# Optimization experiments

Hardware: AMD Instinct MI355X
Metric: run time of the kernel (lower is better)

The kernel has to match this reference:

```python
import jax, jax.numpy as jnp
import numpy as np
import math

B, C, N, M = 4, 128, 4096, 4096

def setup_inputs() -> dict:
    key = jax.random.key(0)
    ks = jax.random.split(key, 8)
    return {
        "x1": jax.random.normal(ks[0], (B, C, N), dtype=jnp.float32),
        "p1": jax.random.normal(ks[1], (B, 3, N), dtype=jnp.float32),
        "x2": jax.random.normal(ks[2], (B, C, M), dtype=jnp.float32),
        "p2": jax.random.normal(ks[3], (B, 3, M), dtype=jnp.float32),
        "Wq": jax.random.normal(ks[4], (C, C), dtype=jnp.float32) * 0.05,
        "Wk": jax.random.normal(ks[5], (C, C), dtype=jnp.float32) * 0.05,
        "Wv": jax.random.normal(ks[6], (C, C), dtype=jnp.float32) * 0.05,
        "Wpos": jax.random.normal(ks[7], (C, 3), dtype=jnp.float32) * 0.05,
    }

def reference(x1, p1, x2, p2, Wq, Wk, Wv, Wpos):
    # Conv1d with kernel_size=1, no bias == per-point matmul over channel dim.
    # NOTE: original forward uses self.pos for BOTH p1 and p2 (pos1 conv unused).
    pos = jnp.einsum('ck,bkn->bcn', Wpos, p1)   # [B,C,N]
    pos1 = jnp.einsum('ck,bkm->bcm', Wpos, p2)  # [B,C,M]
    q = jnp.einsum('dc,bcn->bdn', Wq, x1 + pos)   # [B,C,N]
    k = jnp.einsum('dc,bcm->bdm', Wk, x2 + pos1)  # [B,C,M]
    v = jnp.einsum('dc,bcm->bdm', Wv, x2)         # [B,C,M]
    scale = math.sqrt(q.shape[1])  # sqrt(C) -- q.shape[-2] in (B,C,N) layout
    energy = jnp.einsum('bcn,bcm->bnm', q, k) / scale  # [B,N,M]
    attention = jax.nn.softmax(energy, axis=-1)
    vout = jnp.einsum('bnm,bcm->bnc', attention, v)    # [B,N,C]
    out = jnp.swapaxes(vout, 1, 2) + x1                # [B,C,N] residual
    return jnp.swapaxes(out, 1, 2)                     # [B,N,C]
```

## Files before the change

### kernel.cpp

```cpp
#include <hip/hip_runtime.h>
#include <hip/hip_bf16.h>

#define B_ 4
#define C_ 128
#define N_ 4096
#define M_ 4096

typedef __bf16 bf16;
typedef __bf16 bf16x8 __attribute__((ext_vector_type(8)));
typedef float f32x4 __attribute__((ext_vector_type(4)));
typedef float f32x16 __attribute__((ext_vector_type(16)));

#define MFMA16(a, b, c) __builtin_amdgcn_mfma_f32_16x16x32_bf16(a, b, c, 0, 0, 0)
#define MFMA32(a, b, c) __builtin_amdgcn_mfma_f32_32x32x16_bf16(a, b, c, 0, 0, 0)

__device__ inline void gll16(const bf16* g, bf16* l) {
    __builtin_amdgcn_global_load_lds(
        (const __attribute__((address_space(1))) void*)g,
        (__attribute__((address_space(3))) void*)l, 16, 0, 0);
}

__device__ inline unsigned cvtpk(float a, float b) {
    unsigned r;
    asm("v_cvt_pk_bf16_f32 %0, %1, %2" : "=v"(r) : "v"(a), "v"(b));
    return r;
}

__global__ __launch_bounds__(256) void wcvt_kernel(
    const float* __restrict__ Wq, const float* __restrict__ Wk,
    const float* __restrict__ Wv, bf16* __restrict__ Wb) {
    int i = (blockIdx.x * 256 + threadIdx.x) * 4;
    const float* src = (i < 16384) ? Wq : (i < 32768) ? Wk : Wv;
    int off = i & 16383;
    float4 v = *(const float4*)(src + off);
    union { ushort4 u4; bf16 h[4]; } pk;
    pk.h[0] = (bf16)v.x; pk.h[1] = (bf16)v.y;
    pk.h[2] = (bf16)v.z; pk.h[3] = (bf16)v.w;
    *(ushort4*)(Wb + i) = pk.u4;
}

__global__ __launch_bounds__(768) void proj_kernel(
    const float* __restrict__ x1, const float* __restrict__ p1,
    const float* __restrict__ x2, const float* __restrict__ p2,
    const bf16* __restrict__ Wb, const float* __restrict__ Wpos,
    bf16* __restrict__ Qt, bf16* __restrict__ Kt, bf16* __restrict__ Vt) {
    __shared__ __align__(16) bf16 xp1[64 * 136];
    __shared__ __align__(16) bf16 xp2[64 * 136];
    __shared__ __align__(16) bf16 xr2[64 * 136];
    __shared__ float pp1[3 * 64], pp2[3 * 64], wls[384];

    const int t = threadIdx.x;
    const int b = blockIdx.y;
    const int n0 = blockIdx.x * 64;

    if (t < 48) {
        int k3 = t / 16, i4 = (t & 15) * 4;
        *(float4*)&pp1[k3 * 64 + i4] = *(const float4*)(p1 + ((size_t)b * 3 + k3) * N_ + n0 + i4);
    } else if (t < 96) {
        int tt = t - 48;
        int k3 = tt / 16, i4 = (tt & 15) * 4;
        *(float4*)&pp2[k3 * 64 + i4] = *(const float4*)(p2 + ((size_t)b * 3 + k3) * N_ + n0 + i4);
    } else if (t < 192) {
        int i4 = (t - 96) * 4;
        *(float4*)&wls[i4] = *(const float4*)(Wpos + i4);
    }
    __syncthreads();

    for (int s = t; s < 2048; s += 768) {
        int c = s >> 4, n4 = (s & 15) * 4;
        float4 xv = *(const float4*)(x1 + ((size_t)b * C_ + c) * N_ + n0 + n4);
        float w0 = wls[c * 3 + 0], w1 = wls[c * 3 + 1], w2 = wls[c * 3 + 2];
        const float* xa = &xv.x;
        #pragma unroll
        for (int j = 0; j < 4; ++j) {
            float pos = w0 * pp1[n4 + j] + w1 * pp1[64 + n4 + j] + w2 * pp1[128 + n4 + j];
            xp1[(n4 + j) * 136 + c] = (bf16)(xa[j] + pos);
        }
    }
    for (int s = t; s < 2048; s += 768) {
        int c = s >> 4, n4 = (s & 15) * 4;
        float4 xv = *(const float4*)(x2 + ((size_t)b * C_ + c) * N_ + n0 + n4);
        float w0 = wls[c * 3 + 0], w1 = wls[c * 3 + 1], w2 = wls[c * 3 + 2];
        const float* xa = &xv.x;
        #pragma unroll
        for (int j = 0; j < 4; ++j) {
            float pos = w0 * pp2[n4 + j] + w1 * pp2[64 + n4 + j] + w2 * pp2[128 + n4 + j];
            xp2[(n4 + j) * 136 + c] = (bf16)(xa[j] + pos);
            xr2[(n4 + j) * 136 + c] = (bf16)xa[j];
        }
    }
    __syncthreads();

    const int w = t >> 6;
    const int lane = t & 63;
    const int col = lane & 15, quad = lane >> 4;
    const int role = w >> 2, band = w & 3;
    const int nl = band * 16 + col;
    const int n = n0 + nl;

    const bf16* src = (role == 0) ? xp1 : (role == 1) ? xp2 : xr2;
    const bf16* Wm = Wb + role * 16384;

    bf16x8 bx[4];
    #pragma unroll
    for (int cs = 0; cs < 4; ++cs)
        bx[cs] = *(const bf16x8*)&src[nl * 136 + cs * 32 + quad * 8];

    #pragma unroll
    for (int dt = 0; dt < 8; ++dt) {
        f32x4 acc = {0.f, 0.f, 0.f, 0.f};
        #pragma unroll
        for (int cs = 0; cs < 4; ++cs) {
            bf16x8 wf = *(const bf16x8*)(Wm + (dt * 16 + col) * 128 + cs * 32 + quad * 8);
            acc = MFMA16(wf, bx[cs], acc);
        }
        if (role < 2) {
            bf16* Ot = (role == 0) ? Qt : Kt;
            union { ushort4 u4; bf16 h[4]; } pk;
            #pragma unroll
            for (int r = 0; r < 4; ++r) pk.h[r] = (bf16)acc[r];
            *(ushort4*)(Ot + ((size_t)b * N_ + n) * C_ + dt * 16 + quad * 4) = pk.u4;
        } else {
            #pragma unroll
            for (int r = 0; r < 4; ++r)
                Vt[((size_t)b * C_ + dt * 16 + quad * 4 + r) * (size_t)M_ + n] = (bf16)acc[r];
        }
    }
}

__global__ __launch_bounds__(512) void attn_kernel(
    const bf16* __restrict__ Qt, const bf16* __restrict__ Kt,
    const bf16* __restrict__ Vt, const float* __restrict__ x1,
    float* __restrict__ out) {
    __shared__ __align__(16) char smem[132096];

    const int t = threadIdx.x;
    const int w = t >> 6;
    const int lane = t & 63;
    const int col = lane & 31;
    const int hi = lane >> 5;
    const int kg = w & 3;
    const int qg = w >> 2;

    const int g0 = blockIdx.x;
    const int xcd = g0 & 7;
    const int b = xcd >> 1;
    const int qt = (xcd & 1) + ((g0 >> 3) << 1);
    const int n0 = qt * 64;

    const float KS = 0.12752107168406815f;

    const bf16* Kbase = Kt + (size_t)b * M_ * C_;
    const bf16* Vbase = Vt + (size_t)b * C_ * M_;

    bf16x8 qf[8];
    {
        const bf16* Qb = Qt + ((size_t)b * N_ + n0 + qg * 32 + col) * C_ + hi * 8;
        #pragma unroll
        for (int cs = 0; cs < 8; ++cs)
            qf[cs] = *(const bf16x8*)(Qb + cs * 16);
    }

    f32x16 oacc[4];
    #pragma unroll
    for (int i = 0; i < 4; ++i)
        #pragma unroll
        for (int j = 0; j < 16; ++j) oacc[i][j] = 0.f;
    float lacc = 0.f;

    const int key_l = (kg << 5) + col;
    const int kxor = (key_l & 15) << 4;

    const bf16* kpp[4];
    const bf16* vpp[4];
    #pragma unroll
    for (int i = 0; i < 4; ++i) {
        int g = ((w << 2) + i) * 64 + lane;
        int row = g >> 4;
        int sp = (g & 15) ^ (row & 15);
        kpp[i] = Kbase + (size_t)row * C_ + sp * 8;
        vpp[i] = Vbase + (size_t)row * M_ + sp * 8;
    }

    auto stageK = [&](char* dst) {
        #pragma unroll
        for (int i = 0; i < 4; ++i) {
            gll16(kpp[i], (bf16*)dst + ((w << 2) + i) * 512);
            kpp[i] += 128 * C_;
        }
    };
    auto stageV = [&](char* dst) {
        #pragma unroll
        for (int i = 0; i < 4; ++i) {
            gll16(vpp[i], (bf16*)dst + ((w << 2) + i) * 512);
            vpp[i] += 128;
        }
    };

    stageK(smem);
    stageV(smem + 65536);
    stageK(smem + 32768);

    f32x16 sA0, sA1, sB0, sB1;

    auto qkc = [&](const char* kbBuf, f32x16& T0, f32x16& T1) {
        #pragma unroll
        for (int q = 0; q < 16; ++q) { T0[q] = 0.f; T1[q] = 0.f; }
        const char* kbp = kbBuf + key_l * 256;
        __builtin_amdgcn_s_setprio(1);
        #pragma unroll
        for (int cs = 0; cs < 4; ++cs) {
            bf16x8 kf = *(const bf16x8*)(kbp + ((((cs << 1) + hi) << 4) ^ kxor));
            T0 = MFMA32(kf, qf[cs], T0);
        }
        #pragma unroll
        for (int cs = 4; cs < 8; ++cs) {
            bf16x8 kf = *(const bf16x8*)(kbp + ((((cs << 1) + hi) << 4) ^ kxor));
            T1 = MFMA32(kf, qf[cs], T1);
        }
        __builtin_amdgcn_s_setprio(0);
    };

    auto smpv = [&](f32x16& S0, f32x16& S1, const char* vbBuf) {
        float p[16];
        #pragma unroll
        for (int r = 0; r < 16; ++r) {
            float e = fminf((S0[r] + S1[r]) * KS, 60.f);
            p[r] = __builtin_amdgcn_exp2f(e);
        }
        {
            float s01 = (p[0] + p[1]) + (p[2] + p[3]);
            float s23 = (p[4] + p[5]) + (p[6] + p[7]);
            float s45 = (p[8] + p[9]) + (p[10] + p[11]);
            float s67 = (p[12] + p[13]) + (p[14] + p[15]);
            lacc += (s01 + s23) + (s45 + s67);
        }
        unsigned W0 = cvtpk(p[0], p[1]),  W1 = cvtpk(p[2], p[3]);
        unsigned W2 = cvtpk(p[4], p[5]),  W3 = cvtpk(p[6], p[7]);
        unsigned W4 = cvtpk(p[8], p[9]),  W5 = cvtpk(p[10], p[11]);
        unsigned W6 = cvtpk(p[12], p[13]), W7 = cvtpk(p[14], p[15]);
        unsigned X0 = hi ? W0 : W2, X1 = hi ? W1 : W3;
        unsigned Y0 = hi ? W4 : W6, Y1 = hi ? W5 : W7;
        X0 = __shfl_xor(X0, 32, 64);  X1 = __shfl_xor(X1, 32, 64);
        Y0 = __shfl_xor(Y0, 32, 64);  Y1 = __shfl_xor(Y1, 32, 64);
        uint4 u0, u1;
        u0.x = hi ? X0 : W0;  u0.y = hi ? X1 : W1;
        u0.z = hi ? W2 : X0;  u0.w = hi ? W3 : X1;
        u1.x = hi ? Y0 : W4;  u1.y = hi ? Y1 : W5;
        u1.z = hi ? W6 : Y0;  u1.w = hi ? W7 : Y1;
        bf16x8 af0 = __builtin_bit_cast(bf16x8, u0);
        bf16x8 af1 = __builtin_bit_cast(bf16x8, u1);

        __builtin_amdgcn_s_setprio(1);
        #pragma unroll
        for (int ct = 0; ct < 4; ++ct) {
            int c = (ct << 5) + col;
            const char* vbp = vbBuf + c * 256;
            int vxor = (c & 15) << 4;
            bf16x8 vf0 = *(const bf16x8*)(vbp + ((((kg << 2) + hi) << 4) ^ vxor));
            bf16x8 vf1 = *(const bf16x8*)(vbp + ((((kg << 2) + 2 + hi) << 4) ^ vxor));
            oacc[ct] = MFMA32(af0, vf0, oacc[ct]);
            oacc[ct] = MFMA32(af1, vf1, oacc[ct]);
        }
        __builtin_amdgcn_s_setprio(0);
    };

    asm volatile("s_waitcnt vmcnt(8)" ::: "memory");
    __builtin_amdgcn_sched_barrier(0);
    __builtin_amdgcn_s_barrier();
    __builtin_amdgcn_sched_barrier(0);
    qkc(smem, sA0, sA1);

    for (int jp = 0; jp < 16; ++jp) {
        const int j0 = jp * 2, j1 = j0 + 1;

        asm volatile("s_waitcnt vmcnt(0)" ::: "memory");
        __builtin_amdgcn_sched_barrier(0);
        __builtin_amdgcn_s_barrier();
        __builtin_amdgcn_sched_barrier(0);
        if (j0 < 31) stageV(smem + 98304);
        if (j0 < 30) stageK(smem);
        if (j0 < 31) qkc(smem + 32768, sB0, sB1);
        smpv(sA0, sA1, smem + 65536);
        asm volatile("s_waitcnt lgkmcnt(0)" ::: "memory");
        __builtin_amdgcn_sched_barrier(0);

        asm volatile("s_waitcnt vmcnt(0)" ::: "memory");
        __builtin_amdgcn_sched_barrier(0);
        __builtin_amdgcn_s_barrier();
        __builtin_amdgcn_sched_barrier(0);
        if (j1 < 31) stageV(smem + 65536);
        if (j1 < 30) stageK(smem + 32768);
        if (j1 < 31) qkc(smem, sA0, sA1);
        smpv(sB0, sB1, smem + 98304);
        asm volatile("s_waitcnt lgkmcnt(0)" ::: "memory");
        __builtin_amdgcn_sched_barrier(0);
    }

    __builtin_amdgcn_s_barrier();

    float* obuf = (float*)smem;
    float* lps  = (float*)(smem + 131072);

    lacc += __shfl_xor(lacc, 32, 64);
    if (hi == 0) lps[(kg << 6) + (qg << 5) + col] = lacc;

    #pragma unroll
    for (int ct = 0; ct < 4; ++ct)
        #pragma unroll
        for (int r = 0; r < 16; ++r) {
            int q = (r & 3) + ((r >> 2) << 3) + (hi << 2);
            obuf[kg * 8192 + ((qg << 5) + q) * 128 + (ct << 5) + col] = oacc[ct][r];
        }
    __syncthreads();

    const int c2 = lane << 1;
    #pragma unroll
    for (int j = 0; j < 8; ++j) {
        int q = (w << 3) + j;
        float s0 = 0.f, s1 = 0.f;
        #pragma unroll
        for (int pp = 0; pp < 4; ++pp) {
            float2 v = *(const float2*)&obuf[pp * 8192 + q * 128 + c2];
            s0 += v.x; s1 += v.y;
        }
        float lsum = lps[q] + lps[64 + q] + lps[128 + q] + lps[192 + q];
        float linv = 1.0f / lsum;
        int n = n0 + q;
        float o0 = s0 * linv + x1[((size_t)b * C_ + c2) * N_ + n];
        float o1 = s1 * linv + x1[((size_t)b * C_ + c2 + 1) * N_ + n];
        *(float2*)&out[((size_t)b * N_ + n) * C_ + c2] = make_float2(o0, o1);
    }
}

extern "C" void kernel_launch(void* const* d_in, const int* in_sizes, int n_in,
                              void* d_out, int out_size, void* d_ws, size_t ws_size,
                              hipStream_t stream) {
    const float* x1   = (const float*)d_in[0];
    const float* p1   = (const float*)d_in[1];
    const float* x2   = (const float*)d_in[2];
    const float* p2   = (const float*)d_in[3];
    const float* Wq   = (const float*)d_in[4];
    const float* Wk   = (const float*)d_in[5];
    const float* Wv   = (const float*)d_in[6];
    const float* Wpos = (const float*)d_in[7];
    float* out = (float*)d_out;

    bf16* Qt = (bf16*)d_ws;
    bf16* Kt = Qt + (size_t)B_ * N_ * C_;
    bf16* Vt = Kt + (size_t)B_ * M_ * C_;

    bf16* Wb = (bf16*)d_out;

    wcvt_kernel<<<dim3(48), dim3(256), 0, stream>>>(Wq, Wk, Wv, Wb);
    proj_kernel<<<dim3(64, B_), dim3(768), 0, stream>>>(
        x1, p1, x2, p2, Wb, Wpos, Qt, Kt, Vt);
    attn_kernel<<<dim3(256), dim3(512), 0, stream>>>(Qt, Kt, Vt, x1, out);
}
```

Baseline: 143.9 us.

## Split projection kernel into per-role blocks via grid z dimension

The Q/K/V projection kernel now launches a separate 256-thread block for each of Q, K and V instead of one 768-thread block that computes all three. Each block stages only its own input tile in shared memory, so shared-memory use per block drops and more blocks can run at once. The x2 tile is now loaded twice, once by the K blocks and once by the V blocks. For Q and K the MFMA operands are swapped, so each lane writes single bf16 values at stride C instead of packed 4-element stores, which may scatter the global writes.

Measured after the change: 143.8 us. About the same (-0.0%).

```diff
diff --git a/kernel.cpp b/kernel.cpp
--- a/kernel.cpp
+++ b/kernel.cpp
@@ -39,54 +39,51 @@
     *(ushort4*)(Wb + i) = pk.u4;
 }
 
-__global__ __launch_bounds__(768) void proj_kernel(
+__global__ __launch_bounds__(256) void proj_kernel(
     const float* __restrict__ x1, const float* __restrict__ p1,
     const float* __restrict__ x2, const float* __restrict__ p2,
     const bf16* __restrict__ Wb, const float* __restrict__ Wpos,
     bf16* __restrict__ Qt, bf16* __restrict__ Kt, bf16* __restrict__ Vt) {
-    __shared__ __align__(16) bf16 xp1[64 * 136];
-    __shared__ __align__(16) bf16 xp2[64 * 136];
-    __shared__ __align__(16) bf16 xr2[64 * 136];
-    __shared__ float pp1[3 * 64], pp2[3 * 64], wls[384];
+    __shared__ __align__(16) bf16 xt[64 * 136];
+    __shared__ float pp[3 * 64], wls[384];
 
     const int t = threadIdx.x;
     const int b = blockIdx.y;
+    const int role = blockIdx.z;
     const int n0 = blockIdx.x * 64;
 
-    if (t < 48) {
-        int k3 = t / 16, i4 = (t & 15) * 4;
-        *(float4*)&pp1[k3 * 64 + i4] = *(const float4*)(p1 + ((size_t)b * 3 + k3) * N_ + n0 + i4);
-    } else if (t < 96) {
-        int tt = t - 48;
-        int k3 = tt / 16, i4 = (tt & 15) * 4;
-        *(float4*)&pp2[k3 * 64 + i4] = *(const float4*)(p2 + ((size_t)b * 3 + k3) * N_ + n0 + i4);
-    } else if (t < 192) {
-        int i4 = (t - 96) * 4;
-        *(float4*)&wls[i4] = *(const float4*)(Wpos + i4);
+    const float* xs = (role == 0) ? x1 : x2;
+    const float* ps = (role == 0) ? p1 : p2;
+
+    if (role < 2) {
+        if (t < 48) {
+            int k3 = t / 16, i4 = (t & 15) * 4;
+            *(float4*)&pp[k3 * 64 + i4] =
+                *(const float4*)(ps + ((size_t)b * 3 + k3) * N_ + n0 + i4);
+        } else if (t < 144) {
+            int i4 = (t - 48) * 4;
+            *(float4*)&wls[i4] = *(const float4*)(Wpos + i4);
+        }
     }
     __syncthreads();
 
-    for (int s = t; s < 2048; s += 768) {
+    #pragma unroll
+    for (int k = 0; k < 8; ++k) {
+        int s = t + k * 256;
         int c = s >> 4, n4 = (s & 15) * 4;
-        float4 xv = *(const float4*)(x1 + ((size_t)b * C_ + c) * N_ + n0 + n4);
-        float w0 = wls[c * 3 + 0], w1 = wls[c * 3 + 1], w2 = wls[c * 3 + 2];
+        float4 xv = *(const float4*)(xs + ((size_t)b * C_ + c) * N_ + n0 + n4);
         const float* xa = &xv.x;
-        #pragma unroll
-        for (int j = 0; j < 4; ++j) {
-            float pos = w0 * pp1[n4 + j] + w1 * pp1[64 + n4 + j] + w2 * pp1[128 + n4 + j];
-            xp1[(n4 + j) * 136 + c] = (bf16)(xa[j] + pos);
-        }
-    }
-    for (int s = t; s < 2048; s += 768) {
-        int c = s >> 4, n4 = (s & 15) * 4;
-        float4 xv = *(const float4*)(x2 + ((size_t)b * C_ + c) * N_ + n0 + n4);
-        float w0 = wls[c * 3 + 0], w1 = wls[c * 3 + 1], w2 = wls[c * 3 + 2];
-        const float* xa = &xv.x;
-        #pragma unroll
-        for (int j = 0; j < 4; ++j) {
-            float pos = w0 * pp2[n4 + j] + w1 * pp2[64 + n4 + j] + w2 * pp2[128 + n4 + j];
-            xp2[(n4 + j) * 136 + c] = (bf16)(xa[j] + pos);
-            xr2[(n4 + j) * 136 + c] = (bf16)xa[j];
+        if (role < 2) {
+            float w0 = wls[c * 3 + 0], w1 = wls[c * 3 + 1], w2 = wls[c * 3 + 2];
+            #pragma unroll
+            for (int j = 0; j < 4; ++j) {
+                float pos = w0 * pp[n4 + j] + w1 * pp[64 + n4 + j] + w2 * pp[128 + n4 + j];
+                xt[(n4 + j) * 136 + c] = (bf16)(xa[j] + pos);
+            }
+        } else {
+            #pragma unroll
+            for (int j = 0; j < 4; ++j)
+                xt[(n4 + j) * 136 + c] = (bf16)xa[j];
         }
     }
     __syncthreads();
@@ -94,36 +91,43 @@
     const int w = t >> 6;
     const int lane = t & 63;
     const int col = lane & 15, quad = lane >> 4;
-    const int role = w >> 2, band = w & 3;
-    const int nl = band * 16 + col;
-    const int n = n0 + nl;
-
-    const bf16* src = (role == 0) ? xp1 : (role == 1) ? xp2 : xr2;
+    const int nl = w * 16 + col;
+
     const bf16* Wm = Wb + role * 16384;
 
     bf16x8 bx[4];
     #pragma unroll
     for (int cs = 0; cs < 4; ++cs)
-        bx[cs] = *(const bf16x8*)&src[nl * 136 + cs * 32 + quad * 8];
-
-    #pragma unroll
-    for (int dt = 0; dt < 8; ++dt) {
-        f32x4 acc = {0.f, 0.f, 0.f, 0.f};
-        #pragma unroll
-        for (int cs = 0; cs < 4; ++cs) {
-            bf16x8 wf = *(const bf16x8*)(Wm + (dt * 16 + col) * 128 + cs * 32 + quad * 8);
-            acc = MFMA16(wf, bx[cs], acc);
-        }
-        if (role < 2) {
-            bf16* Ot = (role == 0) ? Qt : Kt;
-            union { ushort4 u4; bf16 h[4]; } pk;
-            #pragma unroll
-            for (int r = 0; r < 4; ++r) pk.h[r] = (bf16)acc[r];
-            *(ushort4*)(Ot + ((size_t)b * N_ + n) * C_ + dt * 16 + quad * 4) = pk.u4;
-        } else {
+        bx[cs] = *(const bf16x8*)&xt[nl * 136 + cs * 32 + quad * 8];
+
+    if (role < 2) {
+        bf16* Ot = (role == 0) ? Qt : Kt;
+        #pragma unroll
+        for (int dt = 0; dt < 8; ++dt) {
+            f32x4 acc = {0.f, 0.f, 0.f, 0.f};
+            #pragma unroll
+            for (int cs = 0; cs < 4; ++cs) {
+                bf16x8 wf = *(const bf16x8*)(Wm + (dt * 16 + col) * 128 + cs * 32 + quad * 8);
+                acc = MFMA16(bx[cs], wf, acc);
+            }
+            #pragma unroll
+            for (int r = 0; r < 4; ++r) {
+                int n = n0 + w * 16 + quad * 4 + r;
+                Ot[((size_t)b * N_ + n) * C_ + dt * 16 + col] = (bf16)acc[r];
+            }
+        }
+    } else {
+        #pragma unroll
+        for (int dt = 0; dt < 8; ++dt) {
+            f32x4 acc = {0.f, 0.f, 0.f, 0.f};
+            #pragma unroll
+            for (int cs = 0; cs < 4; ++cs) {
+                bf16x8 wf = *(const bf16x8*)(Wm + (dt * 16 + col) * 128 + cs * 32 + quad * 8);
+                acc = MFMA16(wf, bx[cs], acc);
+            }
             #pragma unroll
             for (int r = 0; r < 4; ++r)
-                Vt[((size_t)b * C_ + dt * 16 + quad * 4 + r) * (size_t)M_ + n] = (bf16)acc[r];
+                Vt[((size_t)b * C_ + dt * 16 + quad * 4 + r) * (size_t)M_ + n0 + nl] = (bf16)acc[r];
         }
     }
 }
@@ -353,7 +357,7 @@
     bf16* Wb = (bf16*)d_out;
 
     wcvt_kernel<<<dim3(48), dim3(256), 0, stream>>>(Wq, Wk, Wv, Wb);
-    proj_kernel<<<dim3(64, B_), dim3(768), 0, stream>>>(
+    proj_kernel<<<dim3(64, B_, 3), dim3(256), 0, stream>>>(
         x1, p1, x2, p2, Wb, Wpos, Qt, Kt, Vt);
     attn_kernel<<<dim3(256), dim3(512), 0, stream>>>(Qt, Kt, Vt, x1, out);
 }
```
